# Performance work log

Measured on AMD Instinct MI355X. Metric: run time of the kernel, lower is better.

## Reference

```python
import jax, jax.numpy as jnp
import numpy as np

B, N, DIM = 8, 4096, 128

def setup_inputs() -> dict:
    key = jax.random.key(0)
    ks = jax.random.split(key, 6)
    s = 1.0 / np.sqrt(DIM)
    return {
        "x": jax.random.normal(ks[0], (B, N, DIM), dtype=jnp.float32),
        "q_global": jax.random.normal(ks[1], (B, N, DIM), dtype=jnp.float32),
        "Wkv": jax.random.normal(ks[2], (DIM, 2 * DIM), dtype=jnp.float32) * s,
        "bkv": jax.random.normal(ks[3], (2 * DIM,), dtype=jnp.float32) * 0.02,
        "Wp": jax.random.normal(ks[4], (DIM, DIM), dtype=jnp.float32) * s,
        "bp": jax.random.normal(ks[5], (DIM,), dtype=jnp.float32) * 0.02,
    }

def reference(x, q_global, Wkv, bkv, Wp, bp):
    # x: [B, n, dim]; kv linear -> split into k, v (each [B, n, dim])
    kv = x @ Wkv + bkv
    k, v = jnp.split(kv, 2, axis=-1)
    dim = x.shape[-1]
    q = q_global * (1.0 / jnp.sqrt(jnp.asarray(dim, x.dtype)))
    # scores = k @ q^T : [B, n, m]; softmax over query axis m (as in source)
    scores = jnp.einsum("bnd,bmd->bnm", k, q)
    attn = jax.nn.softmax(scores, axis=-1)
    # attention @ v : contracts m against v's row index (m == n)
    out = jnp.einsum("bnm,bmd->bnd", attn, v)
    return out @ Wp + bp
```

## Files before the change

### kernel.cpp

```cpp
#include <hip/hip_runtime.h>

typedef __bf16 bf16x8 __attribute__((ext_vector_type(8)));
typedef float f32x4 __attribute__((ext_vector_type(4)));
typedef float f32x16 __attribute__((ext_vector_type(16)));

struct alignas(16) US8 { unsigned short us[8]; };

static __device__ inline unsigned short f2bf(float f) {
  union { float f; unsigned u; } v; v.f = f;
  unsigned r = v.u + 0x7fffu + ((v.u >> 16) & 1u);
  return (unsigned short)(r >> 16);
}

static __device__ inline void gload16(const unsigned short* g, unsigned short* l) {
  __builtin_amdgcn_global_load_lds(
      (const __attribute__((address_space(1))) void*)g,
      (__attribute__((address_space(3))) void*)l, 16, 0, 0);
}

#define NSEQ 4096
#define DIM 128
#define ROWS 32768
#define KH 2

#define EXPC (1.4426950408889634f * 0.08838834764831845f)

__global__ void prep_kernel(const float* __restrict__ Wkv, const float* __restrict__ Wp,
                            unsigned short* __restrict__ wkvT, unsigned short* __restrict__ wpT) {
  const int t = threadIdx.x;
  const int d = (t & 63) * 2;
  if (blockIdx.x < 64) {
    const int col = blockIdx.x * 4 + (t >> 6);
    unsigned short lo = f2bf(Wkv[d * 256 + col]);
    unsigned short hi = f2bf(Wkv[(d + 1) * 256 + col]);
    *reinterpret_cast<unsigned*>(&wkvT[col * 128 + d]) = (unsigned)lo | ((unsigned)hi << 16);
  } else {
    const int col = (blockIdx.x - 64) * 4 + (t >> 6);
    unsigned short lo = f2bf(Wp[d * 128 + col]);
    unsigned short hi = f2bf(Wp[(d + 1) * 128 + col]);
    *reinterpret_cast<unsigned*>(&wpT[col * 128 + d]) = (unsigned)lo | ((unsigned)hi << 16);
  }
}

__global__ __launch_bounds__(256, 2) void kv_kernel(
    const float* __restrict__ x, const unsigned short* __restrict__ wkvT,
    const float* __restrict__ bkv, const float* __restrict__ q,
    unsigned short* __restrict__ kout, unsigned short* __restrict__ vtout,
    unsigned short* __restrict__ qo) {
  const int tid = threadIdx.x;
  if (blockIdx.x >= 512) {
    int i = ((blockIdx.x - 512) * 256 + tid) * 8;
    const float4* p = reinterpret_cast<const float4*>(q + i);
    float4 a = p[0], b = p[1];
    US8 o;
    o.us[0]=f2bf(a.x*EXPC); o.us[1]=f2bf(a.y*EXPC); o.us[2]=f2bf(a.z*EXPC); o.us[3]=f2bf(a.w*EXPC);
    o.us[4]=f2bf(b.x*EXPC); o.us[5]=f2bf(b.y*EXPC); o.us[6]=f2bf(b.z*EXPC); o.us[7]=f2bf(b.w*EXPC);
    int row = i >> 7, d0 = i & 127;
    int bb = row >> 12, n = row & (NSEQ - 1), tile = n >> 6, l = n & 63, kc = d0 >> 3;
    *reinterpret_cast<US8*>(qo + (size_t)bb * NSEQ * DIM + tile * 8192 + kc * 512 + l * 8) = o;
    return;
  }
  __shared__ __align__(16) unsigned short WT[256 * 136];
  const int wv = tid >> 6, lane = tid & 63, l16 = lane & 15, quad = lane >> 4;
  const int row0 = blockIdx.x * 64;

  for (int p = 0; p < 16; ++p) {
    int c = p * 256 + tid;
    int col = c >> 4, c16 = c & 15;
    *reinterpret_cast<US8*>(&WT[col * 136 + c16 * 8]) =
        *reinterpret_cast<const US8*>(wkvT + col * 128 + c16 * 8);
  }
  __syncthreads();

  bf16x8 afrag[4];
  const int arow = row0 + wv * 16 + l16;
  for (int s = 0; s < 4; ++s) {
    const float4* xp = reinterpret_cast<const float4*>(x + (size_t)arow * DIM + s * 32 + quad * 8);
    float4 u0 = xp[0], u1 = xp[1];
    US8 af;
    af.us[0]=f2bf(u0.x); af.us[1]=f2bf(u0.y); af.us[2]=f2bf(u0.z); af.us[3]=f2bf(u0.w);
    af.us[4]=f2bf(u1.x); af.us[5]=f2bf(u1.y); af.us[6]=f2bf(u1.z); af.us[7]=f2bf(u1.w);
    afrag[s] = __builtin_bit_cast(bf16x8, af);
  }
  f32x4 acc[16];
  for (int g = 0; g < 16; ++g) acc[g] = f32x4{0.f, 0.f, 0.f, 0.f};
  for (int s = 0; s < 4; ++s)
    for (int g = 0; g < 16; ++g) {
      bf16x8 bfr = *reinterpret_cast<const bf16x8*>(&WT[(g * 16 + l16) * 136 + s * 32 + quad * 8]);
      acc[g] = __builtin_amdgcn_mfma_f32_16x16x32_bf16(afrag[s], bfr, acc[g], 0, 0, 0);
    }

  for (int g = 0; g < 8; ++g) {
    float bias = bkv[g * 16 + l16];
    for (int r = 0; r < 4; ++r) {
      int orow = row0 + wv * 16 + quad * 4 + r;
      kout[(size_t)orow * DIM + g * 16 + l16] = f2bf(acc[g][r] + bias);
    }
  }
  __syncthreads();
  unsigned short* LDSt = WT;
  for (int g = 0; g < 8; ++g) {
    float bias = bkv[128 + g * 16 + l16];
    for (int r = 0; r < 4; ++r)
      LDSt[(g * 16 + l16) * 72 + wv * 16 + quad * 4 + r] = f2bf(acc[g + 8][r] + bias);
  }
  __syncthreads();
  const int bb = row0 >> 12;
  const int tile = (row0 & (NSEQ - 1)) >> 6;
  unsigned short* vbo = vtout + (size_t)bb * NSEQ * DIM + (size_t)tile * 8192;
  for (int p = 0; p < 4; ++p) {
    int c = p * 256 + tid;
    int idx = c >> 6, l = c & 63;
    int mg = idx >> 1, dh = idx & 1, d = dh * 64 + l;
    int nb = (mg >> 1) * 16 + (mg & 1) * 4;
    uint2 lo = *reinterpret_cast<const uint2*>(&LDSt[d * 72 + nb]);
    uint2 hi = *reinterpret_cast<const uint2*>(&LDSt[d * 72 + nb + 8]);
    uint4 o{lo.x, lo.y, hi.x, hi.y};
    *reinterpret_cast<uint4*>(vbo + (size_t)idx * 512 + l * 8) = o;
  }
}

__global__ __launch_bounds__(256, 2) void attn_kernel(
    const unsigned short* __restrict__ kbuf, const unsigned short* __restrict__ qblk,
    const unsigned short* __restrict__ vblk,
    float* __restrict__ opart, float* __restrict__ lpart) {
  __shared__ __align__(16) unsigned short SH[32768];
  const int tid = threadIdx.x;
  const int wv = tid >> 6, lane = tid & 63, l32 = lane & 31, h = lane >> 5;
  const int b = blockIdx.x & 7;
  const int t = blockIdx.x >> 3;
  const int q0 = (t & 31) * 128;
  const int kh = t >> 5;
  const int key0 = kh * (NSEQ / KH);
  const unsigned short* kb = kbuf + (size_t)b * NSEQ * DIM;
  const unsigned short* qb = qblk + (size_t)b * NSEQ * DIM;
  const unsigned short* vb = vblk + (size_t)b * NSEQ * DIM;

  const unsigned short* gsrc[8];
  int lofs[8];
#pragma unroll
  for (int c = 0; c < 8; ++c) {
    const int idx = wv * 8 + c;
    const unsigned short* p = (idx < 16) ? (qb + idx * 512) : (vb + (size_t)(idx - 16) * 512);
    gsrc[c] = p + (size_t)(key0 >> 6) * 8192 + lane * 8;
    lofs[c] = idx * 512;
  }

  constexpr int NT = NSEQ / KH / 64;
#pragma unroll
  for (int c = 0; c < 8; ++c) gload16(gsrc[c], &SH[lofs[c]]);

  bf16x8 kfrag[8];
  for (int ks = 0; ks < 8; ++ks)
    kfrag[ks] = __builtin_bit_cast(bf16x8, *reinterpret_cast<const US8*>(
        kb + (size_t)(q0 + wv * 32 + l32) * DIM + ks * 16 + h * 8));

  US8 one8;
#pragma unroll
  for (int j = 0; j < 8; ++j) one8.us[j] = 0x3F80;
  const bf16x8 vones = __builtin_bit_cast(bf16x8, one8);

  f32x16 Oacc[4];
  for (int dt = 0; dt < 4; ++dt)
    for (int i = 0; i < 16; ++i) Oacc[dt][i] = 0.f;
  f32x16 Lacc;
  for (int i = 0; i < 16; ++i) Lacc[i] = 0.f;

  __syncthreads();

  for (int it = 0; it < NT; ++it) {
    const int cur = (it & 1) << 14;
    if (it + 1 < NT) {
      const int nxt = cur ^ 16384;
#pragma unroll
      for (int c = 0; c < 8; ++c)
        gload16(gsrc[c] + (size_t)(it + 1) * 8192, &SH[nxt + lofs[c]]);
    }
    const unsigned short* Ksh = SH + cur;
    const unsigned short* Vsh = Ksh + 8192;

    f32x16 S0, S1;
    for (int i = 0; i < 16; ++i) { S0[i] = 0.f; S1[i] = 0.f; }
    __builtin_amdgcn_s_setprio(1);
#pragma unroll
    for (int ks = 0; ks < 8; ++ks) {
      const unsigned short* kc = &Ksh[(ks * 2 + h) * 512];
      bf16x8 a0 = *reinterpret_cast<const bf16x8*>(&kc[l32 * 8]);
      bf16x8 a1 = *reinterpret_cast<const bf16x8*>(&kc[(32 + l32) * 8]);
      S0 = __builtin_amdgcn_mfma_f32_32x32x16_bf16(a0, kfrag[ks], S0, 0, 0, 0);
      S1 = __builtin_amdgcn_mfma_f32_32x32x16_bf16(a1, kfrag[ks], S1, 0, 0, 0);
    }
    __builtin_amdgcn_s_setprio(0);

    bf16x8 pf[2][2];
#pragma unroll
    for (int T = 0; T < 2; ++T) {
      unsigned pk[8];
#pragma unroll
      for (int i2 = 0; i2 < 8; ++i2) {
        float e0 = __builtin_amdgcn_exp2f(T ? S1[i2 * 2] : S0[i2 * 2]);
        float e1 = __builtin_amdgcn_exp2f(T ? S1[i2 * 2 + 1] : S0[i2 * 2 + 1]);
        pk[i2] = __builtin_amdgcn_perm(__builtin_bit_cast(unsigned, e1),
                                       __builtin_bit_cast(unsigned, e0), 0x07060302u);
      }
      pf[T][0] = __builtin_bit_cast(bf16x8, uint4{pk[0], pk[1], pk[2], pk[3]});
      pf[T][1] = __builtin_bit_cast(bf16x8, uint4{pk[4], pk[5], pk[6], pk[7]});
    }

    __builtin_amdgcn_s_setprio(1);
#pragma unroll
    for (int T = 0; T < 2; ++T)
#pragma unroll
      for (int s = 0; s < 2; ++s) {
        const int mg = 4 * T + 2 * s + h;
#pragma unroll
        for (int dt = 0; dt < 4; ++dt) {
          bf16x8 bv = *reinterpret_cast<const bf16x8*>(
              &Vsh[(mg * 2 + (dt >> 1)) * 512 + ((dt & 1) * 32 + l32) * 8]);
          Oacc[dt] = __builtin_amdgcn_mfma_f32_32x32x16_bf16(pf[T][s], bv, Oacc[dt], 0, 0, 0);
        }
        Lacc = __builtin_amdgcn_mfma_f32_32x32x16_bf16(pf[T][s], vones, Lacc, 0, 0, 0);
      }
    __builtin_amdgcn_s_setprio(0);

    __syncthreads();
  }

#pragma unroll
  for (int i = 0; i < 16; ++i) {
    int n = (i & 3) + 8 * (i >> 2) + 4 * h;
    if (l32 == n)
      lpart[(size_t)kh * ROWS + (size_t)b * NSEQ + q0 + wv * 32 + n] = Lacc[i];
  }
  float* ob = opart + (size_t)kh * ROWS * DIM + ((size_t)b * NSEQ + q0 + wv * 32) * DIM;
  for (int dt = 0; dt < 4; ++dt)
    for (int i = 0; i < 16; ++i) {
      int n = (i & 3) + 8 * (i >> 2) + 4 * h;
      ob[n * DIM + dt * 32 + l32] = Oacc[dt][i];
    }
}

__global__ __launch_bounds__(256, 2) void combine_proj_kernel(
    const float* __restrict__ opart, const float* __restrict__ lpart,
    const unsigned short* __restrict__ wpT, const float* __restrict__ bp,
    float* __restrict__ out) {
  __shared__ __align__(16) unsigned short WT[128 * 136];
  const int tid = threadIdx.x;
  const int wv = tid >> 6, lane = tid & 63, l16 = lane & 15, quad = lane >> 4;
  const int row0 = blockIdx.x * 64;

  for (int p = 0; p < 8; ++p) {
    int c = p * 256 + tid;
    int col = c >> 4, c16 = c & 15;
    *reinterpret_cast<US8*>(&WT[col * 136 + c16 * 8]) =
        *reinterpret_cast<const US8*>(wpT + col * 128 + c16 * 8);
  }
  __syncthreads();

  f32x4 acc[8];
  for (int g = 0; g < 8; ++g) acc[g] = f32x4{0.f, 0.f, 0.f, 0.f};
  const int arow = row0 + wv * 16 + l16;
  float linv = 1.f / (lpart[arow] + lpart[ROWS + arow]);
  for (int s = 0; s < 4; ++s) {
    const size_t base = (size_t)arow * DIM + s * 32 + quad * 8;
    float4 s0 = *reinterpret_cast<const float4*>(opart + base);
    float4 s1 = *reinterpret_cast<const float4*>(opart + base + 4);
    float4 u0 = *reinterpret_cast<const float4*>(opart + (size_t)ROWS * DIM + base);
    float4 u1 = *reinterpret_cast<const float4*>(opart + (size_t)ROWS * DIM + base + 4);
    US8 af;
    af.us[0]=f2bf((s0.x+u0.x)*linv); af.us[1]=f2bf((s0.y+u0.y)*linv);
    af.us[2]=f2bf((s0.z+u0.z)*linv); af.us[3]=f2bf((s0.w+u0.w)*linv);
    af.us[4]=f2bf((s1.x+u1.x)*linv); af.us[5]=f2bf((s1.y+u1.y)*linv);
    af.us[6]=f2bf((s1.z+u1.z)*linv); af.us[7]=f2bf((s1.w+u1.w)*linv);
    bf16x8 a = __builtin_bit_cast(bf16x8, af);
    for (int g = 0; g < 8; ++g) {
      bf16x8 bfr = *reinterpret_cast<const bf16x8*>(&WT[(g * 16 + l16) * 136 + s * 32 + quad * 8]);
      acc[g] = __builtin_amdgcn_mfma_f32_16x16x32_bf16(a, bfr, acc[g], 0, 0, 0);
    }
  }
  for (int g = 0; g < 8; ++g) {
    float bias = bp[g * 16 + l16];
    for (int r = 0; r < 4; ++r) {
      int orow = row0 + wv * 16 + quad * 4 + r;
      out[(size_t)orow * DIM + g * 16 + l16] = acc[g][r] + bias;
    }
  }
}

extern "C" void kernel_launch(void* const* d_in, const int* in_sizes, int n_in,
                              void* d_out, int out_size, void* d_ws, size_t ws_size,
                              hipStream_t stream) {
  (void)in_sizes; (void)n_in; (void)out_size; (void)ws_size;
  const float* x   = (const float*)d_in[0];
  const float* qg  = (const float*)d_in[1];
  const float* Wkv = (const float*)d_in[2];
  const float* bkv = (const float*)d_in[3];
  const float* Wp  = (const float*)d_in[4];
  const float* bp  = (const float*)d_in[5];
  float* out = (float*)d_out;

  unsigned short* qbf  = (unsigned short*)d_ws;
  unsigned short* kbf  = qbf + (size_t)ROWS * DIM;
  unsigned short* vtbf = kbf + (size_t)ROWS * DIM;
  unsigned short* wkvT = vtbf + (size_t)ROWS * DIM;
  unsigned short* wpT  = wkvT + 256 * 128;
  float* lpart = (float*)(wpT + 128 * 128);
  float* opart = lpart + (size_t)KH * ROWS;

  hipLaunchKernelGGL(prep_kernel, dim3(96), dim3(256), 0, stream, Wkv, Wp, wkvT, wpT);
  hipLaunchKernelGGL(kv_kernel, dim3(512 + 2048), dim3(256), 0, stream,
                     x, wkvT, bkv, qg, kbf, vtbf, qbf);
  hipLaunchKernelGGL(attn_kernel, dim3(8 * 32 * KH), dim3(256), 0, stream, kbf, qbf, vtbf, opart, lpart);
  hipLaunchKernelGGL(combine_proj_kernel, dim3(ROWS / 64), dim3(256), 0, stream, opart, lpart, wpT, bp, out);
}
```

Measured before the change: 172.6 us.

## Split keys four ways, single-buffer attention LDS, separate q cast kernel

Raises the key-split factor from 2 to 4, doubling the attention grid. Halves the attention shared memory by dropping double buffering in favour of a load-sync-compute loop, and raises launch bounds to 4 blocks per CU for more occupancy. The q bf16 cast moves into its own kernel, and the combine step now sums KH partials. The trade-off is no copy/compute overlap inside a block, plus twice the partial-output traffic (fp32 O partials) written and read by combine.

```diff
diff --git a/kernel.cpp b/kernel.cpp
--- a/kernel.cpp
+++ b/kernel.cpp
@@ -21,7 +21,7 @@
 #define NSEQ 4096
 #define DIM 128
 #define ROWS 32768
-#define KH 2
+#define KH 4
 
 #define EXPC (1.4426950408889634f * 0.08838834764831845f)
 
@@ -42,24 +42,24 @@
   }
 }
 
+__global__ __launch_bounds__(256, 8) void qcast_kernel(
+    const float* __restrict__ q, unsigned short* __restrict__ qo) {
+  int i = (blockIdx.x * 256 + threadIdx.x) * 8;
+  const float4* p = reinterpret_cast<const float4*>(q + i);
+  float4 a = p[0], b = p[1];
+  US8 o;
+  o.us[0]=f2bf(a.x*EXPC); o.us[1]=f2bf(a.y*EXPC); o.us[2]=f2bf(a.z*EXPC); o.us[3]=f2bf(a.w*EXPC);
+  o.us[4]=f2bf(b.x*EXPC); o.us[5]=f2bf(b.y*EXPC); o.us[6]=f2bf(b.z*EXPC); o.us[7]=f2bf(b.w*EXPC);
+  int row = i >> 7, d0 = i & 127;
+  int bb = row >> 12, n = row & (NSEQ - 1), tile = n >> 6, l = n & 63, kc = d0 >> 3;
+  *reinterpret_cast<US8*>(qo + (size_t)bb * NSEQ * DIM + tile * 8192 + kc * 512 + l * 8) = o;
+}
+
 __global__ __launch_bounds__(256, 2) void kv_kernel(
     const float* __restrict__ x, const unsigned short* __restrict__ wkvT,
-    const float* __restrict__ bkv, const float* __restrict__ q,
-    unsigned short* __restrict__ kout, unsigned short* __restrict__ vtout,
-    unsigned short* __restrict__ qo) {
+    const float* __restrict__ bkv,
+    unsigned short* __restrict__ kout, unsigned short* __restrict__ vtout) {
   const int tid = threadIdx.x;
-  if (blockIdx.x >= 512) {
-    int i = ((blockIdx.x - 512) * 256 + tid) * 8;
-    const float4* p = reinterpret_cast<const float4*>(q + i);
-    float4 a = p[0], b = p[1];
-    US8 o;
-    o.us[0]=f2bf(a.x*EXPC); o.us[1]=f2bf(a.y*EXPC); o.us[2]=f2bf(a.z*EXPC); o.us[3]=f2bf(a.w*EXPC);
-    o.us[4]=f2bf(b.x*EXPC); o.us[5]=f2bf(b.y*EXPC); o.us[6]=f2bf(b.z*EXPC); o.us[7]=f2bf(b.w*EXPC);
-    int row = i >> 7, d0 = i & 127;
-    int bb = row >> 12, n = row & (NSEQ - 1), tile = n >> 6, l = n & 63, kc = d0 >> 3;
-    *reinterpret_cast<US8*>(qo + (size_t)bb * NSEQ * DIM + tile * 8192 + kc * 512 + l * 8) = o;
-    return;
-  }
   __shared__ __align__(16) unsigned short WT[256 * 136];
   const int wv = tid >> 6, lane = tid & 63, l16 = lane & 15, quad = lane >> 4;
   const int row0 = blockIdx.x * 64;
@@ -120,11 +120,13 @@
   }
 }
 
-__global__ __launch_bounds__(256, 2) void attn_kernel(
+__global__ __launch_bounds__(256, 4) void attn_kernel(
     const unsigned short* __restrict__ kbuf, const unsigned short* __restrict__ qblk,
     const unsigned short* __restrict__ vblk,
     float* __restrict__ opart, float* __restrict__ lpart) {
-  __shared__ __align__(16) unsigned short SH[32768];
+  __shared__ __align__(16) unsigned short SH[16384];
+  unsigned short* Ksh = SH;
+  unsigned short* Vsh = SH + 8192;
   const int tid = threadIdx.x;
   const int wv = tid >> 6, lane = tid & 63, l32 = lane & 31, h = lane >> 5;
   const int b = blockIdx.x & 7;
@@ -146,10 +148,6 @@
     lofs[c] = idx * 512;
   }
 
-  constexpr int NT = NSEQ / KH / 64;
-#pragma unroll
-  for (int c = 0; c < 8; ++c) gload16(gsrc[c], &SH[lofs[c]]);
-
   bf16x8 kfrag[8];
   for (int ks = 0; ks < 8; ++ks)
     kfrag[ks] = __builtin_bit_cast(bf16x8, *reinterpret_cast<const US8*>(
@@ -166,18 +164,13 @@
   f32x16 Lacc;
   for (int i = 0; i < 16; ++i) Lacc[i] = 0.f;
 
-  __syncthreads();
-
+  constexpr int NT = NSEQ / KH / 64;
   for (int it = 0; it < NT; ++it) {
-    const int cur = (it & 1) << 14;
-    if (it + 1 < NT) {
-      const int nxt = cur ^ 16384;
-#pragma unroll
-      for (int c = 0; c < 8; ++c)
-        gload16(gsrc[c] + (size_t)(it + 1) * 8192, &SH[nxt + lofs[c]]);
-    }
-    const unsigned short* Ksh = SH + cur;
-    const unsigned short* Vsh = Ksh + 8192;
+    __syncthreads();
+#pragma unroll
+    for (int c = 0; c < 8; ++c)
+      gload16(gsrc[c] + (size_t)it * 8192, &SH[lofs[c]]);
+    __syncthreads();
 
     f32x16 S0, S1;
     for (int i = 0; i < 16; ++i) { S0[i] = 0.f; S1[i] = 0.f; }
@@ -222,8 +215,6 @@
         Lacc = __builtin_amdgcn_mfma_f32_32x32x16_bf16(pf[T][s], vones, Lacc, 0, 0, 0);
       }
     __builtin_amdgcn_s_setprio(0);
-
-    __syncthreads();
   }
 
 #pragma unroll
@@ -260,18 +251,25 @@
   f32x4 acc[8];
   for (int g = 0; g < 8; ++g) acc[g] = f32x4{0.f, 0.f, 0.f, 0.f};
   const int arow = row0 + wv * 16 + l16;
-  float linv = 1.f / (lpart[arow] + lpart[ROWS + arow]);
+  float lsum = 0.f;
+#pragma unroll
+  for (int p = 0; p < KH; ++p) lsum += lpart[(size_t)p * ROWS + arow];
+  float linv = 1.f / lsum;
   for (int s = 0; s < 4; ++s) {
     const size_t base = (size_t)arow * DIM + s * 32 + quad * 8;
-    float4 s0 = *reinterpret_cast<const float4*>(opart + base);
-    float4 s1 = *reinterpret_cast<const float4*>(opart + base + 4);
-    float4 u0 = *reinterpret_cast<const float4*>(opart + (size_t)ROWS * DIM + base);
-    float4 u1 = *reinterpret_cast<const float4*>(opart + (size_t)ROWS * DIM + base + 4);
+    float4 s0{0.f,0.f,0.f,0.f}, s1{0.f,0.f,0.f,0.f};
+#pragma unroll
+    for (int p = 0; p < KH; ++p) {
+      float4 u0 = *reinterpret_cast<const float4*>(opart + (size_t)p * ROWS * DIM + base);
+      float4 u1 = *reinterpret_cast<const float4*>(opart + (size_t)p * ROWS * DIM + base + 4);
+      s0.x += u0.x; s0.y += u0.y; s0.z += u0.z; s0.w += u0.w;
+      s1.x += u1.x; s1.y += u1.y; s1.z += u1.z; s1.w += u1.w;
+    }
     US8 af;
-    af.us[0]=f2bf((s0.x+u0.x)*linv); af.us[1]=f2bf((s0.y+u0.y)*linv);
-    af.us[2]=f2bf((s0.z+u0.z)*linv); af.us[3]=f2bf((s0.w+u0.w)*linv);
-    af.us[4]=f2bf((s1.x+u1.x)*linv); af.us[5]=f2bf((s1.y+u1.y)*linv);
-    af.us[6]=f2bf((s1.z+u1.z)*linv); af.us[7]=f2bf((s1.w+u1.w)*linv);
+    af.us[0]=f2bf(s0.x*linv); af.us[1]=f2bf(s0.y*linv);
+    af.us[2]=f2bf(s0.z*linv); af.us[3]=f2bf(s0.w*linv);
+    af.us[4]=f2bf(s1.x*linv); af.us[5]=f2bf(s1.y*linv);
+    af.us[6]=f2bf(s1.z*linv); af.us[7]=f2bf(s1.w*linv);
     bf16x8 a = __builtin_bit_cast(bf16x8, af);
     for (int g = 0; g < 8; ++g) {
       bf16x8 bfr = *reinterpret_cast<const bf16x8*>(&WT[(g * 16 + l16) * 136 + s * 32 + quad * 8]);
@@ -308,8 +306,8 @@
   float* opart = lpart + (size_t)KH * ROWS;
 
   hipLaunchKernelGGL(prep_kernel, dim3(96), dim3(256), 0, stream, Wkv, Wp, wkvT, wpT);
-  hipLaunchKernelGGL(kv_kernel, dim3(512 + 2048), dim3(256), 0, stream,
-                     x, wkvT, bkv, qg, kbf, vtbf, qbf);
+  hipLaunchKernelGGL(qcast_kernel, dim3(2048), dim3(256), 0, stream, qg, qbf);
+  hipLaunchKernelGGL(kv_kernel, dim3(512), dim3(256), 0, stream, x, wkvT, bkv, kbf, vtbf);
   hipLaunchKernelGGL(attn_kernel, dim3(8 * 32 * KH), dim3(256), 0, stream, kbf, qbf, vtbf, opart, lpart);
   hipLaunchKernelGGL(combine_proj_kernel, dim3(ROWS / 64), dim3(256), 0, stream, opart, lpart, wpT, bp, out);
 }
```

Result: slower. 264.4 us (+53.2%).
